# Optimization experiments

Hardware: AMD Instinct MI355X
Metric: run time of the kernel (lower is better)

Reference implementation:

```python
import jax, jax.numpy as jnp
import numpy as np

NUM_EMB = 1_000_000
EMB_DIM = 64
ATT_DIM = 64
NUM_BAGS = 16384
BAG_LEN = 50  # total indices = NUM_BAGS * BAG_LEN = 819200


def setup_inputs() -> dict:
    key = jax.random.key(0)
    k1, k2, k3, k4, k5 = jax.random.split(key, 5)
    N = NUM_BAGS * BAG_LEN
    input_ = jax.random.randint(k1, (N,), 0, NUM_EMB, dtype=jnp.int64)
    # CSR indptr: fixed-size bags of BAG_LEN (sorted, starts at 0)
    offsets = (jnp.arange(NUM_BAGS, dtype=jnp.int64) * BAG_LEN)
    emb_weight = jax.random.normal(k2, (NUM_EMB, EMB_DIM), dtype=jnp.float32) * 0.05
    proj_w = jax.random.normal(k3, (ATT_DIM, EMB_DIM), dtype=jnp.float32) * (1.0 / np.sqrt(EMB_DIM))
    proj_b = jax.random.normal(k4, (ATT_DIM,), dtype=jnp.float32) * 0.01
    att_h = jax.random.normal(k5, (ATT_DIM,), dtype=jnp.float32) * 0.01
    return {"input_": input_, "offsets": offsets, "emb_weight": emb_weight,
            "proj_w": proj_w, "proj_b": proj_b, "att_h": att_h}


def reference(input_, offsets, emb_weight, proj_w, proj_b, att_h):
    N = input_.shape[0]
    B = offsets.shape[0]
    # Gather embedding rows once; reused for both attention logits and pooling.
    att_emb = emb_weight[input_]                                  # [N, D]
    # logits = tanh(emb @ W^T + b) . att_h
    att = jnp.einsum('na,a->n', jnp.tanh(att_emb @ proj_w.T + proj_b), att_h)  # [N]
    # segment id for each index from CSR indptr (repeat_interleave equivalent)
    seg = jnp.searchsorted(offsets, jnp.arange(N), side='right') - 1           # [N]
    # stable segment softmax over ragged bags
    m = jax.ops.segment_max(att, seg, num_segments=B)            # [B]
    e = jnp.exp(att - m[seg])                                    # [N]
    s = jax.ops.segment_sum(e, seg, num_segments=B)              # [B]
    w = e / s[seg]                                               # [N]
    # attention-weighted sum pooling (embedding_bag with per_sample_weights)
    return jax.ops.segment_sum(w[:, None] * att_emb, seg, num_segments=B)     # [B, D]
```

## Files before the change

### kernel.cpp

```cpp
#include <hip/hip_runtime.h>
#include <hip/hip_bf16.h>
#include <math.h>

#define EMB_DIM 64
#define MAXL    64

typedef __attribute__((ext_vector_type(8))) short  bf16x8;
typedef __attribute__((ext_vector_type(8))) ushort u16x8;
typedef __attribute__((ext_vector_type(4))) float  f32x4;

static __device__ __forceinline__ ushort f2bf(float x) {
    __hip_bfloat16 h = __float2bfloat16(x);
    return __builtin_bit_cast(ushort, h);
}
static __device__ __forceinline__ float bf2f(ushort u) {
    return __uint_as_float(((unsigned)u) << 16);
}
static __device__ __forceinline__ bf16x8 pack8(float4 a, float4 b) {
    bf16x8 r;
    r[0] = (short)f2bf(a.x); r[1] = (short)f2bf(a.y);
    r[2] = (short)f2bf(a.z); r[3] = (short)f2bf(a.w);
    r[4] = (short)f2bf(b.x); r[5] = (short)f2bf(b.y);
    r[6] = (short)f2bf(b.z); r[7] = (short)f2bf(b.w);
    return r;
}

__global__ void convert_w_kernel(const float* __restrict__ proj_w,
                                 ushort* __restrict__ w_bf) {
    int t = blockIdx.x * 256 + threadIdx.x;
    if (t < EMB_DIM * EMB_DIM) w_bf[t] = f2bf(proj_w[t]);
}

__global__ __launch_bounds__(256, 4)
void pooled_attn_mlp(const int* __restrict__ input_,
                     const int* __restrict__ offsets,
                     const float* __restrict__ emb,
                     const ushort* __restrict__ w_bf,
                     const float* __restrict__ proj_b,
                     const float* __restrict__ att_h,
                     float* __restrict__ out,
                     int n_bags, int n_total)
{
    __shared__ ushort Wl[512 * 8];
    __shared__ float  Att[4][MAXL];

    const int tid  = threadIdx.x;
    const int lane = tid & 63;
    const int wv   = tid >> 6;
    const int c    = lane & 15;
    const int rg   = lane >> 4;

    #pragma unroll
    for (int k = tid; k < 512; k += 256) {
        const int blk = k >> 6;
        const int ln  = k & 63;
        const int cc  = ln & 15, rr = ln >> 4;
        const int t   = blk >> 1, s = blk & 1;
        *(u16x8*)&Wl[(size_t)k * 8] =
            *(const u16x8*)&w_bf[(cc + 16 * t) * EMB_DIM + s * 32 + rr * 8];
    }
    float bbias[4], hval[4];
    #pragma unroll
    for (int t = 0; t < 4; ++t) {
        bbias[t] = proj_b[c + 16 * t];
        hval[t]  = att_h[c + 16 * t];
    }
    __syncthreads();

    const int b = blockIdx.x * 4 + wv;
    if (b >= n_bags) return;
    float* att = Att[wv];

    const int s0 = offsets[b];
    const int e1 = (b + 1 < n_bags) ? offsets[b + 1] : n_total;
    int L = e1 - s0; L = L < 0 ? 0 : (L > MAXL ? MAXL : L);
    const int myidx = (lane < L) ? input_[s0 + lane] : 0;

    float4 st[16];
    #pragma unroll
    for (int chl = 0; chl < 4; ++chl) {
        const int row  = 16 * chl + c;
        const int ridx = __shfl(myidx, row, 64);
        const float4* rp = (const float4*)(emb + (size_t)ridx * EMB_DIM);
        st[chl * 4 + 0] = rp[rg * 2 + 0];
        st[chl * 4 + 1] = rp[rg * 2 + 1];
        st[chl * 4 + 2] = rp[8 + rg * 2 + 0];
        st[chl * 4 + 3] = rp[8 + rg * 2 + 1];
    }

    bf16x8 ea[4][2];
    ea[0][0] = pack8(st[0], st[1]); ea[0][1] = pack8(st[2], st[3]);
    ea[1][0] = pack8(st[4], st[5]); ea[1][1] = pack8(st[6], st[7]);

    #pragma unroll
    for (int ch = 0; ch < 4; ++ch) {
        if (ch == 2) {
            ea[2][0] = pack8(st[8],  st[9]);  ea[2][1] = pack8(st[10], st[11]);
            ea[3][0] = pack8(st[12], st[13]); ea[3][1] = pack8(st[14], st[15]);
        }
        f32x4 acc[4];
        #pragma unroll
        for (int t = 0; t < 4; ++t) acc[t] = (f32x4){0.f, 0.f, 0.f, 0.f};
        #pragma unroll
        for (int s = 0; s < 2; ++s) {
            #pragma unroll
            for (int t = 0; t < 4; ++t) {
                bf16x8 bbf = *(const bf16x8*)&Wl[((t * 2 + s) * 64 + lane) * 8];
                acc[t] = __builtin_amdgcn_mfma_f32_16x16x32_bf16(ea[ch][s], bbf, acc[t], 0, 0, 0);
            }
        }
        float vatt[4] = {0.f, 0.f, 0.f, 0.f};
        #pragma unroll
        for (int t = 0; t < 4; ++t) {
            #pragma unroll
            for (int r = 0; r < 4; ++r) {
                const float z = acc[t][r] + bbias[t];
                const float u = z * z;
                float p = fmaf(-0.05396825397f, u, 0.1333333333f);
                p = fmaf(p, u, -0.3333333333f);
                p = fmaf(p, u, 1.0f);
                vatt[r] = fmaf(z * p, hval[t], vatt[r]);
            }
        }
        #pragma unroll
        for (int r = 0; r < 4; ++r) {
            float v = vatt[r];
            v += __shfl_xor(v, 1, 16);
            v += __shfl_xor(v, 2, 16);
            v += __shfl_xor(v, 4, 16);
            v += __shfl_xor(v, 8, 16);
            vatt[r] = v;
        }
        if (c == 0) {
            f32x4 v4 = {vatt[0], vatt[1], vatt[2], vatt[3]};
            *(f32x4*)&att[16 * ch + 4 * rg] = v4;
        }
    }

    const float av = (lane < L) ? att[lane] : -INFINITY;
    float m = av;
    #pragma unroll
    for (int o = 32; o; o >>= 1) m = fmaxf(m, __shfl_xor(m, o, 64));
    const float ee = (lane < L) ? __expf(av - m) : 0.0f;
    float ssum = ee;
    #pragma unroll
    for (int o = 32; o; o >>= 1) ssum += __shfl_xor(ssum, o, 64);
    const float wt = ee * (1.0f / ssum);

    float pool[16];
    #pragma unroll
    for (int k = 0; k < 16; ++k) pool[k] = 0.f;
    #pragma unroll
    for (int ch = 0; ch < 4; ++ch) {
        const float wr = __shfl(wt, 16 * ch + c, 64);
        #pragma unroll
        for (int s = 0; s < 2; ++s)
            #pragma unroll
            for (int j = 0; j < 8; ++j)
                pool[s * 8 + j] = fmaf(wr, bf2f((ushort)ea[ch][s][j]), pool[s * 8 + j]);
    }
    #pragma unroll
    for (int o = 1; o < 16; o <<= 1) {
        #pragma unroll
        for (int k = 0; k < 16; ++k) pool[k] += __shfl_xor(pool[k], o, 16);
    }
    if (c == 0) {
        float4* op = (float4*)(out + (size_t)b * EMB_DIM);
        op[rg * 2 + 0]     = make_float4(pool[0],  pool[1],  pool[2],  pool[3]);
        op[rg * 2 + 1]     = make_float4(pool[4],  pool[5],  pool[6],  pool[7]);
        op[8 + rg * 2 + 0] = make_float4(pool[8],  pool[9],  pool[10], pool[11]);
        op[8 + rg * 2 + 1] = make_float4(pool[12], pool[13], pool[14], pool[15]);
    }
}

extern "C" void kernel_launch(void* const* d_in, const int* in_sizes, int n_in,
                              void* d_out, int out_size, void* d_ws, size_t ws_size,
                              hipStream_t stream) {
    const int*   input_  = (const int*)d_in[0];
    const int*   offsets = (const int*)d_in[1];
    const float* emb     = (const float*)d_in[2];
    const float* proj_w  = (const float*)d_in[3];
    const float* proj_b  = (const float*)d_in[4];
    const float* att_h   = (const float*)d_in[5];
    float* out = (float*)d_out;

    const int N = in_sizes[0];
    const int B = in_sizes[1];

    ushort* w_bf = (ushort*)d_ws;

    convert_w_kernel<<<(EMB_DIM * EMB_DIM + 255) / 256, 256, 0, stream>>>(proj_w, w_bf);
    pooled_attn_mlp<<<(B + 3) / 4, 256, 0, stream>>>(
        input_, offsets, emb, w_bf, proj_b, att_h, out, B, N);
}
```

Baseline: 52.63 us.

## Compute transposed MLP tile in registers, drop LDS staging and barrier

Swaps the MFMA operand roles so each wave computes Z^T with the projection weights as the A operand, loaded per lane straight from global memory instead of staged in shared memory. Per-row attention logits then end up owned by the lanes that hold the matching embedding rows, so the LDS Att buffer, the __syncthreads and the weight-shuffle broadcasts go away. Softmax becomes a 16-lane reduction plus per-lane exp. This costs more registers for the weight fragments and a redundant per-wave global (cached) load of W.

```diff
diff --git a/kernel.cpp b/kernel.cpp
--- a/kernel.cpp
+++ b/kernel.cpp
@@ -6,7 +6,6 @@
 #define MAXL    64
 
 typedef __attribute__((ext_vector_type(8))) short  bf16x8;
-typedef __attribute__((ext_vector_type(8))) ushort u16x8;
 typedef __attribute__((ext_vector_type(4))) float  f32x4;
 
 static __device__ __forceinline__ ushort f2bf(float x) {
@@ -32,44 +31,23 @@
 }
 
 __global__ __launch_bounds__(256, 4)
-void pooled_attn_mlp(const int* __restrict__ input_,
-                     const int* __restrict__ offsets,
-                     const float* __restrict__ emb,
-                     const ushort* __restrict__ w_bf,
-                     const float* __restrict__ proj_b,
-                     const float* __restrict__ att_h,
-                     float* __restrict__ out,
-                     int n_bags, int n_total)
+void pooled_attn_zt(const int* __restrict__ input_,
+                    const int* __restrict__ offsets,
+                    const float* __restrict__ emb,
+                    const ushort* __restrict__ w_bf,
+                    const float* __restrict__ proj_b,
+                    const float* __restrict__ att_h,
+                    float* __restrict__ out,
+                    int n_bags, int n_total)
 {
-    __shared__ ushort Wl[512 * 8];
-    __shared__ float  Att[4][MAXL];
-
     const int tid  = threadIdx.x;
     const int lane = tid & 63;
     const int wv   = tid >> 6;
     const int c    = lane & 15;
     const int rg   = lane >> 4;
 
-    #pragma unroll
-    for (int k = tid; k < 512; k += 256) {
-        const int blk = k >> 6;
-        const int ln  = k & 63;
-        const int cc  = ln & 15, rr = ln >> 4;
-        const int t   = blk >> 1, s = blk & 1;
-        *(u16x8*)&Wl[(size_t)k * 8] =
-            *(const u16x8*)&w_bf[(cc + 16 * t) * EMB_DIM + s * 32 + rr * 8];
-    }
-    float bbias[4], hval[4];
-    #pragma unroll
-    for (int t = 0; t < 4; ++t) {
-        bbias[t] = proj_b[c + 16 * t];
-        hval[t]  = att_h[c + 16 * t];
-    }
-    __syncthreads();
-
     const int b = blockIdx.x * 4 + wv;
     if (b >= n_bags) return;
-    float* att = Att[wv];
 
     const int s0 = offsets[b];
     const int e1 = (b + 1 < n_bags) ? offsets[b + 1] : n_total;
@@ -78,86 +56,98 @@
 
     float4 st[16];
     #pragma unroll
-    for (int chl = 0; chl < 4; ++chl) {
-        const int row  = 16 * chl + c;
+    for (int ti = 0; ti < 4; ++ti) {
+        const int row  = 16 * ti + c;
         const int ridx = __shfl(myidx, row, 64);
         const float4* rp = (const float4*)(emb + (size_t)ridx * EMB_DIM);
-        st[chl * 4 + 0] = rp[rg * 2 + 0];
-        st[chl * 4 + 1] = rp[rg * 2 + 1];
-        st[chl * 4 + 2] = rp[8 + rg * 2 + 0];
-        st[chl * 4 + 3] = rp[8 + rg * 2 + 1];
+        st[ti * 4 + 0] = rp[rg * 2 + 0];
+        st[ti * 4 + 1] = rp[rg * 2 + 1];
+        st[ti * 4 + 2] = rp[8 + rg * 2 + 0];
+        st[ti * 4 + 3] = rp[8 + rg * 2 + 1];
+    }
+
+    bf16x8 wf[4][2];
+    #pragma unroll
+    for (int ta = 0; ta < 4; ++ta)
+        #pragma unroll
+        for (int s = 0; s < 2; ++s)
+            wf[ta][s] = *(const bf16x8*)&w_bf[(16 * ta + c) * EMB_DIM + s * 32 + rg * 8];
+
+    float4 hb[4], bv[4];
+    #pragma unroll
+    for (int ta = 0; ta < 4; ++ta) {
+        hb[ta] = *(const float4*)&att_h[16 * ta + 4 * rg];
+        bv[ta] = *(const float4*)&proj_b[16 * ta + 4 * rg];
     }
 
     bf16x8 ea[4][2];
-    ea[0][0] = pack8(st[0], st[1]); ea[0][1] = pack8(st[2], st[3]);
-    ea[1][0] = pack8(st[4], st[5]); ea[1][1] = pack8(st[6], st[7]);
+    #pragma unroll
+    for (int ti = 0; ti < 4; ++ti) {
+        ea[ti][0] = pack8(st[ti * 4 + 0], st[ti * 4 + 1]);
+        ea[ti][1] = pack8(st[ti * 4 + 2], st[ti * 4 + 3]);
+    }
 
+    float patt[4] = {0.f, 0.f, 0.f, 0.f};
     #pragma unroll
-    for (int ch = 0; ch < 4; ++ch) {
-        if (ch == 2) {
-            ea[2][0] = pack8(st[8],  st[9]);  ea[2][1] = pack8(st[10], st[11]);
-            ea[3][0] = pack8(st[12], st[13]); ea[3][1] = pack8(st[14], st[15]);
-        }
+    for (int ta = 0; ta < 4; ++ta) {
         f32x4 acc[4];
         #pragma unroll
-        for (int t = 0; t < 4; ++t) acc[t] = (f32x4){0.f, 0.f, 0.f, 0.f};
+        for (int ti = 0; ti < 4; ++ti) acc[ti] = (f32x4){0.f, 0.f, 0.f, 0.f};
         #pragma unroll
-        for (int s = 0; s < 2; ++s) {
+        for (int s = 0; s < 2; ++s)
             #pragma unroll
-            for (int t = 0; t < 4; ++t) {
-                bf16x8 bbf = *(const bf16x8*)&Wl[((t * 2 + s) * 64 + lane) * 8];
-                acc[t] = __builtin_amdgcn_mfma_f32_16x16x32_bf16(ea[ch][s], bbf, acc[t], 0, 0, 0);
-            }
-        }
-        float vatt[4] = {0.f, 0.f, 0.f, 0.f};
+            for (int ti = 0; ti < 4; ++ti)
+                acc[ti] = __builtin_amdgcn_mfma_f32_16x16x32_bf16(wf[ta][s], ea[ti][s], acc[ti], 0, 0, 0);
         #pragma unroll
-        for (int t = 0; t < 4; ++t) {
+        for (int ti = 0; ti < 4; ++ti) {
             #pragma unroll
             for (int r = 0; r < 4; ++r) {
-                const float z = acc[t][r] + bbias[t];
+                const float z = acc[ti][r] + bv[ta][r];
                 const float u = z * z;
                 float p = fmaf(-0.05396825397f, u, 0.1333333333f);
                 p = fmaf(p, u, -0.3333333333f);
                 p = fmaf(p, u, 1.0f);
-                vatt[r] = fmaf(z * p, hval[t], vatt[r]);
+                patt[ti] = fmaf(z * p, hb[ta][r], patt[ti]);
             }
-        }
-        #pragma unroll
-        for (int r = 0; r < 4; ++r) {
-            float v = vatt[r];
-            v += __shfl_xor(v, 1, 16);
-            v += __shfl_xor(v, 2, 16);
-            v += __shfl_xor(v, 4, 16);
-            v += __shfl_xor(v, 8, 16);
-            vatt[r] = v;
-        }
-        if (c == 0) {
-            f32x4 v4 = {vatt[0], vatt[1], vatt[2], vatt[3]};
-            *(f32x4*)&att[16 * ch + 4 * rg] = v4;
         }
     }
 
-    const float av = (lane < L) ? att[lane] : -INFINITY;
-    float m = av;
     #pragma unroll
-    for (int o = 32; o; o >>= 1) m = fmaxf(m, __shfl_xor(m, o, 64));
-    const float ee = (lane < L) ? __expf(av - m) : 0.0f;
-    float ssum = ee;
+    for (int ti = 0; ti < 4; ++ti) {
+        patt[ti] += __shfl_xor(patt[ti], 16, 64);
+        patt[ti] += __shfl_xor(patt[ti], 32, 64);
+    }
+
+    float m = -INFINITY;
+    float av[4];
     #pragma unroll
-    for (int o = 32; o; o >>= 1) ssum += __shfl_xor(ssum, o, 64);
-    const float wt = ee * (1.0f / ssum);
+    for (int ti = 0; ti < 4; ++ti) {
+        av[ti] = (c + 16 * ti < L) ? patt[ti] : -INFINITY;
+        m = fmaxf(m, av[ti]);
+    }
+    #pragma unroll
+    for (int o = 1; o < 16; o <<= 1) m = fmaxf(m, __shfl_xor(m, o, 16));
+    float ee[4], ssum = 0.f;
+    #pragma unroll
+    for (int ti = 0; ti < 4; ++ti) {
+        ee[ti] = (c + 16 * ti < L) ? __expf(av[ti] - m) : 0.f;
+        ssum += ee[ti];
+    }
+    #pragma unroll
+    for (int o = 1; o < 16; o <<= 1) ssum += __shfl_xor(ssum, o, 16);
+    const float inv = 1.0f / ssum;
 
     float pool[16];
     #pragma unroll
     for (int k = 0; k < 16; ++k) pool[k] = 0.f;
     #pragma unroll
-    for (int ch = 0; ch < 4; ++ch) {
-        const float wr = __shfl(wt, 16 * ch + c, 64);
+    for (int ti = 0; ti < 4; ++ti) {
+        const float wt = ee[ti] * inv;
         #pragma unroll
         for (int s = 0; s < 2; ++s)
             #pragma unroll
             for (int j = 0; j < 8; ++j)
-                pool[s * 8 + j] = fmaf(wr, bf2f((ushort)ea[ch][s][j]), pool[s * 8 + j]);
+                pool[s * 8 + j] = fmaf(wt, bf2f((ushort)ea[ti][s][j]), pool[s * 8 + j]);
     }
     #pragma unroll
     for (int o = 1; o < 16; o <<= 1) {
@@ -165,11 +155,11 @@
         for (int k = 0; k < 16; ++k) pool[k] += __shfl_xor(pool[k], o, 16);
     }
     if (c == 0) {
-        float4* op = (float4*)(out + (size_t)b * EMB_DIM);
-        op[rg * 2 + 0]     = make_float4(pool[0],  pool[1],  pool[2],  pool[3]);
-        op[rg * 2 + 1]     = make_float4(pool[4],  pool[5],  pool[6],  pool[7]);
-        op[8 + rg * 2 + 0] = make_float4(pool[8],  pool[9],  pool[10], pool[11]);
-        op[8 + rg * 2 + 1] = make_float4(pool[12], pool[13], pool[14], pool[15]);
+        float* op = out + (size_t)b * EMB_DIM;
+        *(float4*)&op[8 * rg]          = make_float4(pool[0],  pool[1],  pool[2],  pool[3]);
+        *(float4*)&op[8 * rg + 4]      = make_float4(pool[4],  pool[5],  pool[6],  pool[7]);
+        *(float4*)&op[32 + 8 * rg]     = make_float4(pool[8],  pool[9],  pool[10], pool[11]);
+        *(float4*)&op[32 + 8 * rg + 4] = make_float4(pool[12], pool[13], pool[14], pool[15]);
     }
 }
 
@@ -190,6 +180,6 @@
     ushort* w_bf = (ushort*)d_ws;
 
     convert_w_kernel<<<(EMB_DIM * EMB_DIM + 255) / 256, 256, 0, stream>>>(proj_w, w_bf);
-    pooled_attn_mlp<<<(B + 3) / 4, 256, 0, stream>>>(
+    pooled_attn_zt<<<(B + 3) / 4, 256, 0, stream>>>(
         input_, offsets, emb, w_bf, proj_b, att_h, out, B, N);
 }
```

Result: slower. 66.49 us (+26.3%).
